# Performance work log

Hardware: AMD Instinct MI355X
Metric: run time of the kernel (lower is better)

The kernel has to match this reference:

```python
import jax, jax.numpy as jnp
import numpy as np

HEIGHT = 0.1        # height_factor
MIN_DIST = 10       # min_distance
PROM = 0.05         # prominence_factor


def _find_peaks(xn):
    """scipy.signal.find_peaks(xn, height=HEIGHT, distance=MIN_DIST,
    prominence=PROM) for a single 1D signal, vectorized.
    (Plateau handling omitted: for continuous random inputs exact ties have
    probability zero, so strict local maxima match scipy's _local_maxima_1d.)"""
    N = xn.shape[0]
    pos = jnp.arange(N)

    # 1) strict local maxima (endpoints can never be peaks in scipy)
    interior = (xn[1:-1] > xn[:-2]) & (xn[1:-1] > xn[2:])
    is_peak = jnp.pad(interior, (1, 1), constant_values=False)

    # 2) height filter
    cand = is_peak & (xn >= HEIGHT)

    # 3) distance-based greedy suppression: highest peak first, remove
    #    neighbors with |i-j| < MIN_DIST (matches _select_by_peak_distance)
    order = jnp.argsort(-xn)  # descending by value

    def step(suppressed, idx):
        keep_this = cand[idx] & ~suppressed[idx]
        near = (jnp.abs(pos - idx) < MIN_DIST) & (pos != idx)
        suppressed = suppressed | (keep_this & near)
        return suppressed, keep_this

    _, keeps = jax.lax.scan(step, jnp.zeros(N, dtype=bool), order)
    keep = jnp.zeros(N, dtype=bool).at[order].set(keeps)

    # 4) prominence (wlen=None -> full-signal base search, per position):
    #    left base  = min x over (L, i] where L = last j<i with x[j] > x[i]
    #    right base = min x over [i, R) where R = first j>i with x[j] > x[i]
    greater = xn[None, :] > xn[:, None]              # [i, j]: x_j > x_i
    left_stop = greater & (pos[None, :] < pos[:, None])
    L = jnp.max(jnp.where(left_stop, pos[None, :], -1), axis=1)
    right_stop = greater & (pos[None, :] > pos[:, None])
    R = jnp.min(jnp.where(right_stop, pos[None, :], N), axis=1)

    big = jnp.asarray(jnp.inf, xn.dtype)
    in_l = (pos[None, :] > L[:, None]) & (pos[None, :] <= pos[:, None])
    lmin = jnp.min(jnp.where(in_l, xn[None, :], big), axis=1)
    in_r = (pos[None, :] >= pos[:, None]) & (pos[None, :] < R[:, None])
    rmin = jnp.min(jnp.where(in_r, xn[None, :], big), axis=1)
    prominence = xn - jnp.maximum(lmin, rmin)

    keep = keep & (prominence >= PROM)
    return keep.astype(xn.dtype)


def setup_inputs() -> dict:
    key = jax.random.key(0)
    x = jax.random.normal(key, (16, 2048), dtype=jnp.float32)
    return {"x": x}


def reference(x):
    # per-sample min-max normalization, as in the torch module
    xmin = jnp.min(x, axis=-1, keepdims=True)
    xmax = jnp.max(x, axis=-1, keepdims=True)
    xn = (x - xmin) / (xmax - xmin + 1e-5)
    return jax.vmap(_find_peaks)(xn)
```

## Files before the change

kernel.cpp:

```cpp
#include <hip/hip_runtime.h>

#define N 2048
#define NT 256
#define EL 8
#define HEIGHTF 0.1f
#define PROMF 0.05f
#define LVLS 8

__global__ __launch_bounds__(NT)
void peak_kernel(const float* __restrict__ x, float* __restrict__ out) {
    __shared__ float xs[N];
    __shared__ float actl[16 + N + 24];
    __shared__ unsigned int nk32[3 + NT + 3];
    __shared__ float TMX[LVLS][N];
    __shared__ float TMN[LVLS][N];
    __shared__ float wred[8];
    __shared__ int wtot[4];
    __shared__ unsigned short klist[NT];
    __shared__ unsigned char keepres[N];
    __shared__ int donecnt;

    const int row = blockIdx.x;
    const int t = threadIdx.x;
    const int base = t * EL;
    const float* xr = x + row * (size_t)N;
    const int wv = t >> 6, ln = t & 63;

    float4 Ld0 = ((const float4*)(xr + base))[0];
    float4 Ld1 = ((const float4*)(xr + base))[1];
    float v0[EL] = {Ld0.x, Ld0.y, Ld0.z, Ld0.w, Ld1.x, Ld1.y, Ld1.z, Ld1.w};
    float mn = v0[0], mx = v0[0];
    #pragma unroll
    for (int e = 1; e < EL; ++e) { mn = fminf(mn, v0[e]); mx = fmaxf(mx, v0[e]); }
    #pragma unroll
    for (int off = 32; off > 0; off >>= 1) {
        mn = fminf(mn, __shfl_xor(mn, off, 64));
        mx = fmaxf(mx, __shfl_xor(mx, off, 64));
    }
    if (ln == 0) { wred[wv] = mn; wred[4 + wv] = mx; }
    nk32[t] = 0;
    if (t < 6) nk32[NT + t] = 0;
    if (t == 0) donecnt = 0;
    if (t < 16) actl[t] = -1e30f;
    if (t < 24) actl[16 + N + t] = -1e30f;
    __syncthreads();

    const float xmin = fminf(fminf(wred[0], wred[1]), fminf(wred[2], wred[3]));
    const float xmax = fmaxf(fmaxf(wred[4], wred[5]), fmaxf(wred[6], wred[7]));
    const float den = (xmax - xmin) + 1e-5f;
    float vn[EL];
    #pragma unroll
    for (int e = 0; e < EL; ++e) {
        vn[e] = (v0[e] - xmin) / den;
        xs[base + e] = vn[e];
    }
    __syncthreads();

    unsigned int undec = 0, kept = 0;
    #pragma unroll
    for (int e = 0; e < EL; ++e) {
        int i = base + e;
        float v = vn[e];
        float lf = (e == 0) ? ((i >= 1) ? xs[i-1] : 3e38f) : vn[e-1];
        float rt = (e == EL-1) ? ((i+1 < N) ? xs[i+1] : 3e38f) : vn[e+1];
        bool c = (i >= 1) && (i <= N-2) && (v > lf) && (v > rt) && (v >= HEIGHTF);
        if (c) undec |= (1u << e);
        actl[16 + i] = c ? v : -1e30f;
    }
    __syncthreads();

    float a[40];
    {
        const float4* ap = (const float4*)(actl + base);
        #pragma unroll
        for (int q = 0; q < 10; ++q) {
            float4 w = ap[q];
            a[4*q+0] = w.x; a[4*q+1] = w.y; a[4*q+2] = w.z; a[4*q+3] = w.w;
        }
    }

    auto compute_wins = [&](unsigned int ud) -> unsigned int {
        float m2v[25], m4v[23], m8v[19];
        #pragma unroll
        for (int s = 0; s < 25; ++s) m2v[s] = fmaxf(a[7+s], a[8+s]);
        #pragma unroll
        for (int s = 0; s < 23; ++s) m4v[s] = fmaxf(m2v[s], m2v[s+2]);
        #pragma unroll
        for (int s = 0; s < 19; ++s) m8v[s] = fmaxf(m4v[s], m4v[s+4]);
        unsigned int wb = 0;
        #pragma unroll
        for (int e = 0; e < EL; ++e) {
            if (ud & (1u << e)) {
                float v = a[16+e];
                float wl = fmaxf(m8v[e], a[15+e]);
                float wr = fmaxf(m8v[10+e], a[25+e]);
                if (wl < v && wr <= v) wb |= (1u << e);
            }
        }
        return wb;
    };

    {
        volatile unsigned int* nkv = nk32 + 3;
        volatile int* dcp = (volatile int*)&donecnt;
        unsigned long long lastV = ~0ULL;
        bool counted = false;
        int guard = 0;
        while (true) {
            if (undec) {
                unsigned long long V = 0;
                #pragma unroll
                for (int q = 0; q < 7; ++q)
                    V |= ((unsigned long long)(nkv[t - 3 + q] & 0xFFu)) << (8 * q);
                V <<= 1;
                if (V != lastV) {
                    lastV = V;
                    #pragma unroll
                    for (int s = 0; s < 40; ++s)
                        if ((V >> s) & 0x7FFFFULL) a[s] = -1e30f;
                    #pragma unroll
                    for (int e = 0; e < EL; ++e)
                        if (undec & (1u << e))
                            if ((V >> (16 + e)) & 0x7FFFFULL) undec &= ~(1u << e);
                    if (undec) {
                        unsigned int wb = compute_wins(undec);
                        if (wb) {
                            kept |= wb;
                            undec = 0;
                            nkv[t] = kept;
                        }
                    }
                } else {
                    __builtin_amdgcn_s_sleep(1);
                }
            }
            if (!undec && !counted) {
                nkv[t] = kept;
                __threadfence_block();
                atomicAdd(&donecnt, 1);
                counted = true;
            }
            if (*dcp >= NT) break;
            if (counted) __builtin_amdgcn_s_sleep(2);
            if (++guard > 65536) break;
        }
    }
    __syncthreads();

    float cx[EL], cn[EL];
    #pragma unroll
    for (int j = 0; j < EL; ++j) {
        int i = t + j * NT;
        float a0 = xs[i];
        bool inb = (i + 1 < N);
        float nb = inb ? xs[i + 1] : 0.0f;
        cx[j] = fmaxf(a0, inb ? nb : -3e38f);
        cn[j] = fminf(a0, inb ? nb : 3e38f);
        TMX[0][i] = cx[j];
        TMN[0][i] = cn[j];
    }
    int myc = __popc(kept);
    int pre = myc;
    #pragma unroll
    for (int off = 1; off < 64; off <<= 1) {
        int up = __shfl_up(pre, off, 64);
        if (ln >= off) pre += up;
    }
    if (ln == 63) wtot[wv] = pre;
    #pragma unroll
    for (int e = 0; e < EL; ++e) keepres[base + e] = 0;
    __syncthreads();

    {
        int woff = 0;
        #pragma unroll
        for (int w = 0; w < 4; ++w) woff += (w < wv) ? wtot[w] : 0;
        int slot = woff + pre - myc;
        #pragma unroll
        for (int e = 0; e < EL; ++e)
            if (kept & (1u << e)) klist[slot++] = (unsigned short)(base + e);
    }
    const int ktot = wtot[0] + wtot[1] + wtot[2] + wtot[3];
    #pragma unroll
    for (int pp = 0; pp < 3; ++pp) {
        const int Lv = 1 + 2 * pp;
        const int h = 1 << Lv;
        #pragma unroll
        for (int j = 0; j < EL; ++j) {
            int i = t + j * NT;
            float x1 = (i +   h < N) ? TMX[Lv-1][i+  h] : -3e38f;
            float x2 = (i + 2*h < N) ? TMX[Lv-1][i+2*h] : -3e38f;
            float x3 = (i + 3*h < N) ? TMX[Lv-1][i+3*h] : -3e38f;
            float n1 = (i +   h < N) ? TMN[Lv-1][i+  h] : 3e38f;
            float n2 = (i + 2*h < N) ? TMN[Lv-1][i+2*h] : 3e38f;
            float n3 = (i + 3*h < N) ? TMN[Lv-1][i+3*h] : 3e38f;
            float tx = fmaxf(cx[j], x1), tn = fminf(cn[j], n1);
            TMX[Lv][i] = tx;  TMN[Lv][i] = tn;
            cx[j] = fmaxf(tx, fmaxf(x2, x3));
            cn[j] = fminf(tn, fminf(n2, n3));
            TMX[Lv+1][i] = cx[j];  TMN[Lv+1][i] = cn[j];
        }
        __syncthreads();
    }
    {
        const int h = 128;
        #pragma unroll
        for (int j = 0; j < EL; ++j) {
            int i = t + j * NT;
            float x1 = (i + h < N) ? TMX[6][i+h] : -3e38f;
            float n1 = (i + h < N) ? TMN[6][i+h] : 3e38f;
            cx[j] = fmaxf(cx[j], x1);
            cn[j] = fminf(cn[j], n1);
            TMX[7][i] = cx[j];  TMN[7][i] = cn[j];
        }
        __syncthreads();
    }

    if (t < ktot) {
        const int i = klist[t];
        const float v = xs[i];
        const float* TX0 = &TMX[0][0];
        const float* TN0 = &TMN[0][0];
        int Lph = 0, Lp = i - 1, Lk = 0, Ls = 0;
        float Lm = v;
        if (Lp < 0) Lph = 2;
        int Rph = 0, Rp = i + 1, Rk = 0;
        float Rm = v;
        if (Rp >= N) Rph = 2;
        while (Lph != 2 || Rph != 2) {
            int lLev = 0, lIdx = 0, rLev = 0, rIdx = 0, Lrs = 0;
            if (Lph == 0) {
                int len = Lp + 1;
                Lk = (len >= (1 << LVLS)) ? LVLS : (31 - __clz(len));
                Ls = Lp + 1 - (1 << Lk);
                lLev = Lk - 1; lIdx = Ls;
            } else if (Lph == 1) {
                Lrs = Ls + (1 << (Lk - 1));
                lLev = Lk - 2; lIdx = Lrs;
            }
            if (Rph == 0) {
                int len = N - Rp;
                Rk = (len >= (1 << LVLS)) ? LVLS : (31 - __clz(len));
                rLev = Rk - 1; rIdx = Rp;
            } else if (Rph == 1) {
                rLev = Rk - 2; rIdx = Rp;
            }
            float lx = 0.0f, lnv = 0.0f, rx = 0.0f, rnv = 0.0f;
            if (Lph != 2) {
                const float* bX = (lLev < 0) ? xs : (TX0 + lLev * N);
                const float* bN = (lLev < 0) ? xs : (TN0 + lLev * N);
                lx = bX[lIdx]; lnv = bN[lIdx];
            }
            if (Rph != 2) {
                const float* bX = (rLev < 0) ? xs : (TX0 + rLev * N);
                const float* bN = (rLev < 0) ? xs : (TN0 + rLev * N);
                rx = bX[rIdx]; rnv = bN[rIdx];
            }
            if (Lph == 0) {
                if (lx > v) Lph = (Lk == 0) ? 2 : 1;
                else { Lm = fminf(Lm, lnv); Lp = Ls - 1; if (Lp < 0) Lph = 2; }
            } else if (Lph == 1) {
                if (lx > v) Ls = Lrs; else Lm = fminf(Lm, lnv);
                if (--Lk == 0) Lph = 2;
            }
            if (Rph == 0) {
                if (rx > v) Rph = (Rk == 0) ? 2 : 1;
                else { Rm = fminf(Rm, rnv); Rp += (1 << Rk); if (Rp >= N) Rph = 2; }
            } else if (Rph == 1) {
                if (!(rx > v)) { Rm = fminf(Rm, rnv); Rp += (1 << (Rk - 1)); }
                if (--Rk == 0) Rph = 2;
            }
        }
        if (v - fmaxf(Lm, Rm) >= PROMF) keepres[i] = 1;
    }
    __syncthreads();

    float res[EL];
    #pragma unroll
    for (int e = 0; e < EL; ++e) res[e] = keepres[base + e] ? 1.0f : 0.0f;
    float* outr = out + row * (size_t)N + base;
    ((float4*)outr)[0] = make_float4(res[0], res[1], res[2], res[3]);
    ((float4*)outr)[1] = make_float4(res[4], res[5], res[6], res[7]);
}

extern "C" void kernel_launch(void* const* d_in, const int* in_sizes, int n_in,
                              void* d_out, int out_size, void* d_ws, size_t ws_size,
                              hipStream_t stream) {
    const float* x = (const float*)d_in[0];
    float* outp = (float*)d_out;
    const int rows = in_sizes[0] / N;
    peak_kernel<<<rows, NT, 0, stream>>>(x, outp);
}
```

Measured before the change: 23.24 us.

## Resolve greedy peak suppression locally over wider window before cross-thread polling

Each thread now loads a 56-element window of candidate peaks and repeatedly finds window-local winners, meaning peaks that dominate their ±9 neighborhood, including those in neighbouring threads' ranges. It applies their suppression masks itself, so many decisions resolve without waiting for neighbour threads to publish keep bits. This is meant to cut the number of shared-memory polling rounds and sleeps in the serial dependency chain. The cost is more register pressure from the larger array and extra max-tree work per iteration, and the sleep in the polling loop is removed.

```diff
diff --git a/kernel.cpp b/kernel.cpp
--- a/kernel.cpp
+++ b/kernel.cpp
@@ -10,7 +10,7 @@
 __global__ __launch_bounds__(NT)
 void peak_kernel(const float* __restrict__ x, float* __restrict__ out) {
     __shared__ float xs[N];
-    __shared__ float actl[16 + N + 24];
+    __shared__ float actl[24 + N + 32];
     __shared__ unsigned int nk32[3 + NT + 3];
     __shared__ float TMX[LVLS][N];
     __shared__ float TMN[LVLS][N];
@@ -41,8 +41,8 @@
     nk32[t] = 0;
     if (t < 6) nk32[NT + t] = 0;
     if (t == 0) donecnt = 0;
-    if (t < 16) actl[t] = -1e30f;
-    if (t < 24) actl[16 + N + t] = -1e30f;
+    if (t < 24) actl[t] = -1e30f;
+    if (t < 32) actl[24 + N + t] = -1e30f;
     __syncthreads();
 
     const float xmin = fminf(fminf(wred[0], wred[1]), fminf(wred[2], wred[3]));
@@ -65,73 +65,99 @@
         float rt = (e == EL-1) ? ((i+1 < N) ? xs[i+1] : 3e38f) : vn[e+1];
         bool c = (i >= 1) && (i <= N-2) && (v > lf) && (v > rt) && (v >= HEIGHTF);
         if (c) undec |= (1u << e);
-        actl[16 + i] = c ? v : -1e30f;
-    }
-    __syncthreads();
-
-    float a[40];
+        actl[24 + i] = c ? v : -1e30f;
+    }
+    __syncthreads();
+
+    float a[56];
     {
         const float4* ap = (const float4*)(actl + base);
         #pragma unroll
-        for (int q = 0; q < 10; ++q) {
+        for (int q = 0; q < 14; ++q) {
             float4 w = ap[q];
             a[4*q+0] = w.x; a[4*q+1] = w.y; a[4*q+2] = w.z; a[4*q+3] = w.w;
         }
     }
 
-    auto compute_wins = [&](unsigned int ud) -> unsigned int {
-        float m2v[25], m4v[23], m8v[19];
-        #pragma unroll
-        for (int s = 0; s < 25; ++s) m2v[s] = fmaxf(a[7+s], a[8+s]);
-        #pragma unroll
-        for (int s = 0; s < 23; ++s) m4v[s] = fmaxf(m2v[s], m2v[s+2]);
-        #pragma unroll
-        for (int s = 0; s < 19; ++s) m8v[s] = fmaxf(m4v[s], m4v[s+4]);
-        unsigned int wb = 0;
+    volatile unsigned int* nkv = nk32 + 3;
+
+    auto compute_W = [&]() -> unsigned long long {
+        unsigned long long W = 0;
+        {
+            float m2[37], m4[35];
+            #pragma unroll
+            for (int s2 = 0; s2 < 37; ++s2) m2[s2] = fmaxf(a[s2], a[s2+1]);
+            #pragma unroll
+            for (int s4 = 0; s4 < 35; ++s4) m4[s4] = fmaxf(m2[s4], m2[s4+2]);
+            #pragma unroll
+            for (int s = 9; s < 28; ++s) {
+                float v = a[s];
+                float wl = fmaxf(fmaxf(m4[s-9], m4[s-5]), a[s-1]);
+                float wr = fmaxf(fmaxf(m4[s+1], m4[s+5]), a[s+9]);
+                if (wl < v && wr <= v) W |= (1ULL << s);
+            }
+        }
+        {
+            float m2[36], m4[34];
+            #pragma unroll
+            for (int s2 = 0; s2 < 36; ++s2) m2[s2] = fmaxf(a[19+s2], a[20+s2]);
+            #pragma unroll
+            for (int s4 = 0; s4 < 34; ++s4) m4[s4] = fmaxf(m2[s4], m2[s4+2]);
+            #pragma unroll
+            for (int s = 28; s < 47; ++s) {
+                float v = a[s];
+                float wl = fmaxf(fmaxf(m4[s-28], m4[s-24]), a[s-1]);
+                float wr = fmaxf(fmaxf(m4[s-18], m4[s-14]), a[s+9]);
+                if (wl < v && wr <= v) W |= (1ULL << s);
+            }
+        }
+        return W;
+    };
+
+    auto apply_mask = [&](unsigned long long Wm) {
+        #pragma unroll
+        for (int s = 0; s < 56; ++s) {
+            unsigned long long m = (s >= 9) ? ((Wm >> (s-9)) & 0x7FFFFULL)
+                                            : (Wm & ((1ULL << (s+10)) - 1));
+            if (m) a[s] = -1e30f;
+        }
+        unsigned int oldk = kept;
         #pragma unroll
         for (int e = 0; e < EL; ++e) {
-            if (ud & (1u << e)) {
-                float v = a[16+e];
-                float wl = fmaxf(m8v[e], a[15+e]);
-                float wr = fmaxf(m8v[10+e], a[25+e]);
-                if (wl < v && wr <= v) wb |= (1u << e);
-            }
-        }
-        return wb;
+            if (undec & (1u << e)) {
+                const int s = 24 + e;
+                unsigned long long w19 = (Wm >> (s-9)) & 0x7FFFFULL;
+                if ((w19 >> 9) & 1ULL) { kept |= (1u << e); undec &= ~(1u << e); }
+                else if (w19)          { undec &= ~(1u << e); }
+            }
+        }
+        if (kept != oldk) nkv[t] = kept;
     };
 
+    auto resolve = [&]() {
+        while (true) {
+            unsigned long long W = compute_W();
+            if (!W) break;
+            apply_mask(W);
+        }
+    };
+
     {
-        volatile unsigned int* nkv = nk32 + 3;
         volatile int* dcp = (volatile int*)&donecnt;
-        unsigned long long lastV = ~0ULL;
+        unsigned long long lastV = 0;
         bool counted = false;
         int guard = 0;
+        if (undec) resolve();
         while (true) {
             if (undec) {
                 unsigned long long V = 0;
                 #pragma unroll
                 for (int q = 0; q < 7; ++q)
                     V |= ((unsigned long long)(nkv[t - 3 + q] & 0xFFu)) << (8 * q);
-                V <<= 1;
                 if (V != lastV) {
                     lastV = V;
-                    #pragma unroll
-                    for (int s = 0; s < 40; ++s)
-                        if ((V >> s) & 0x7FFFFULL) a[s] = -1e30f;
-                    #pragma unroll
-                    for (int e = 0; e < EL; ++e)
-                        if (undec & (1u << e))
-                            if ((V >> (16 + e)) & 0x7FFFFULL) undec &= ~(1u << e);
-                    if (undec) {
-                        unsigned int wb = compute_wins(undec);
-                        if (wb) {
-                            kept |= wb;
-                            undec = 0;
-                            nkv[t] = kept;
-                        }
-                    }
-                } else {
-                    __builtin_amdgcn_s_sleep(1);
+                    apply_mask(V);
+                    if (undec) resolve();
                 }
             }
             if (!undec && !counted) {
```

Measured after the change: 75.80 us. 3.26x slower.

## Overlap sparse-table construction with distance-suppression spin loop using per-wave completion flags

Applied to the files above, without the earlier changes.

Interleaves building the min/max sparse-table levels with the iterative peak-distance suppression loop, so table construction fills the idle polling time instead of running as a separate phase afterwards. The block-wide atomic done counter is replaced by per-wave ballot flags. The neighbour-suppression mask is now computed with a bit dilation instead of per-bit window tests, and an initial win check is done before polling. This adds __syncthreads inside the polling loop for the first levels, which couples threads that were previously independent and could add barrier stalls.

```diff
diff --git a/kernel.cpp b/kernel.cpp
--- a/kernel.cpp
+++ b/kernel.cpp
@@ -16,9 +16,9 @@
     __shared__ float TMN[LVLS][N];
     __shared__ float wred[8];
     __shared__ int wtot[4];
+    __shared__ int wdone[4];
     __shared__ unsigned short klist[NT];
     __shared__ unsigned char keepres[N];
-    __shared__ int donecnt;
 
     const int row = blockIdx.x;
     const int t = threadIdx.x;
@@ -40,7 +40,7 @@
     if (ln == 0) { wred[wv] = mn; wred[4 + wv] = mx; }
     nk32[t] = 0;
     if (t < 6) nk32[NT + t] = 0;
-    if (t == 0) donecnt = 0;
+    if (t < 4) wdone[t] = 0;
     if (t < 16) actl[t] = -1e30f;
     if (t < 24) actl[16 + N + t] = -1e30f;
     __syncthreads();
@@ -66,87 +66,8 @@
         bool c = (i >= 1) && (i <= N-2) && (v > lf) && (v > rt) && (v >= HEIGHTF);
         if (c) undec |= (1u << e);
         actl[16 + i] = c ? v : -1e30f;
-    }
-    __syncthreads();
-
-    float a[40];
-    {
-        const float4* ap = (const float4*)(actl + base);
-        #pragma unroll
-        for (int q = 0; q < 10; ++q) {
-            float4 w = ap[q];
-            a[4*q+0] = w.x; a[4*q+1] = w.y; a[4*q+2] = w.z; a[4*q+3] = w.w;
-        }
-    }
-
-    auto compute_wins = [&](unsigned int ud) -> unsigned int {
-        float m2v[25], m4v[23], m8v[19];
-        #pragma unroll
-        for (int s = 0; s < 25; ++s) m2v[s] = fmaxf(a[7+s], a[8+s]);
-        #pragma unroll
-        for (int s = 0; s < 23; ++s) m4v[s] = fmaxf(m2v[s], m2v[s+2]);
-        #pragma unroll
-        for (int s = 0; s < 19; ++s) m8v[s] = fmaxf(m4v[s], m4v[s+4]);
-        unsigned int wb = 0;
-        #pragma unroll
-        for (int e = 0; e < EL; ++e) {
-            if (ud & (1u << e)) {
-                float v = a[16+e];
-                float wl = fmaxf(m8v[e], a[15+e]);
-                float wr = fmaxf(m8v[10+e], a[25+e]);
-                if (wl < v && wr <= v) wb |= (1u << e);
-            }
-        }
-        return wb;
-    };
-
-    {
-        volatile unsigned int* nkv = nk32 + 3;
-        volatile int* dcp = (volatile int*)&donecnt;
-        unsigned long long lastV = ~0ULL;
-        bool counted = false;
-        int guard = 0;
-        while (true) {
-            if (undec) {
-                unsigned long long V = 0;
-                #pragma unroll
-                for (int q = 0; q < 7; ++q)
-                    V |= ((unsigned long long)(nkv[t - 3 + q] & 0xFFu)) << (8 * q);
-                V <<= 1;
-                if (V != lastV) {
-                    lastV = V;
-                    #pragma unroll
-                    for (int s = 0; s < 40; ++s)
-                        if ((V >> s) & 0x7FFFFULL) a[s] = -1e30f;
-                    #pragma unroll
-                    for (int e = 0; e < EL; ++e)
-                        if (undec & (1u << e))
-                            if ((V >> (16 + e)) & 0x7FFFFULL) undec &= ~(1u << e);
-                    if (undec) {
-                        unsigned int wb = compute_wins(undec);
-                        if (wb) {
-                            kept |= wb;
-                            undec = 0;
-                            nkv[t] = kept;
-                        }
-                    }
-                } else {
-                    __builtin_amdgcn_s_sleep(1);
-                }
-            }
-            if (!undec && !counted) {
-                nkv[t] = kept;
-                __threadfence_block();
-                atomicAdd(&donecnt, 1);
-                counted = true;
-            }
-            if (*dcp >= NT) break;
-            if (counted) __builtin_amdgcn_s_sleep(2);
-            if (++guard > 65536) break;
-        }
-    }
-    __syncthreads();
-
+        keepres[i] = 0;
+    }
     float cx[EL], cn[EL];
     #pragma unroll
     for (int j = 0; j < EL; ++j) {
@@ -159,6 +80,107 @@
         TMX[0][i] = cx[j];
         TMN[0][i] = cn[j];
     }
+    __syncthreads();
+
+    float a[40];
+    {
+        const float4* ap = (const float4*)(actl + base);
+        #pragma unroll
+        for (int q = 0; q < 10; ++q) {
+            float4 w = ap[q];
+            a[4*q+0] = w.x; a[4*q+1] = w.y; a[4*q+2] = w.z; a[4*q+3] = w.w;
+        }
+    }
+
+    auto compute_wins = [&](unsigned int ud) -> unsigned int {
+        float m2v[25], m4v[23], m8v[19];
+        #pragma unroll
+        for (int s = 0; s < 25; ++s) m2v[s] = fmaxf(a[7+s], a[8+s]);
+        #pragma unroll
+        for (int s = 0; s < 23; ++s) m4v[s] = fmaxf(m2v[s], m2v[s+2]);
+        #pragma unroll
+        for (int s = 0; s < 19; ++s) m8v[s] = fmaxf(m4v[s], m4v[s+4]);
+        unsigned int wb = 0;
+        #pragma unroll
+        for (int e = 0; e < EL; ++e) {
+            if (ud & (1u << e)) {
+                float v = a[16+e];
+                float wl = fmaxf(m8v[e], a[15+e]);
+                float wr = fmaxf(m8v[10+e], a[25+e]);
+                if (wl < v && wr <= v) wb |= (1u << e);
+            }
+        }
+        return wb;
+    };
+
+    auto dilate9 = [](unsigned long long m) -> unsigned long long {
+        m |= (m << 1) | (m >> 1);
+        m |= (m << 2) | (m >> 2);
+        m |= (m << 3) | (m >> 3);
+        m |= (m << 3) | (m >> 3);
+        return m;
+    };
+
+    {
+        volatile unsigned int* nkv = nk32 + 3;
+        unsigned long long lastV = 0;
+        int lvl = 1;
+        int guard = 0;
+        if (undec) {
+            unsigned int wb = compute_wins(undec);
+            if (wb) { kept |= wb; undec = 0; nkv[t] = kept; }
+        }
+        while (true) {
+            if (undec) {
+                unsigned long long V = 0;
+                #pragma unroll
+                for (int q = 0; q < 7; ++q)
+                    V |= ((unsigned long long)(nkv[t - 3 + q] & 0xFFu)) << (8 * q);
+                if (V != lastV) {
+                    lastV = V;
+                    unsigned long long D = dilate9(V);
+                    #pragma unroll
+                    for (int s = 0; s < 40; ++s)
+                        if ((D >> (s + 8)) & 1ULL) a[s] = -1e30f;
+                    #pragma unroll
+                    for (int e = 0; e < EL; ++e)
+                        if (undec & (1u << e))
+                            if ((D >> (24 + e)) & 1ULL) undec &= ~(1u << e);
+                    if (undec) {
+                        unsigned int wb = compute_wins(undec);
+                        if (wb) { kept |= wb; undec = 0; nkv[t] = kept; }
+                    }
+                }
+            }
+            if (lvl < LVLS) {
+                const int h = 1 << lvl;
+                #pragma unroll
+                for (int j = 0; j < EL; ++j) {
+                    int i = t + j * NT;
+                    bool inb = (i + h < N);
+                    float bx = inb ? TMX[lvl-1][i+h] : -3e38f;
+                    float bn = inb ? TMN[lvl-1][i+h] : 3e38f;
+                    cx[j] = fmaxf(cx[j], bx);
+                    cn[j] = fminf(cn[j], bn);
+                    TMX[lvl][i] = cx[j];
+                    TMN[lvl][i] = cn[j];
+                }
+                ++lvl;
+                __syncthreads();
+                continue;
+            }
+            bool mydone = (undec == 0);
+            unsigned long long bal = __ballot(mydone);
+            if (bal == ~0ULL && ln == 0) ((volatile int*)wdone)[wv] = 1;
+            volatile int* wd = (volatile int*)wdone;
+            int d0 = wd[0], d1 = wd[1], d2 = wd[2], d3 = wd[3];
+            if (d0 & d1 & d2 & d3) break;
+            if (mydone) __builtin_amdgcn_s_sleep(1);
+            if (++guard > 65536) break;
+        }
+    }
+    __syncthreads();
+
     int myc = __popc(kept);
     int pre = myc;
     #pragma unroll
@@ -167,10 +189,7 @@
         if (ln >= off) pre += up;
     }
     if (ln == 63) wtot[wv] = pre;
-    #pragma unroll
-    for (int e = 0; e < EL; ++e) keepres[base + e] = 0;
-    __syncthreads();
-
+    __syncthreads();
     {
         int woff = 0;
         #pragma unroll
@@ -181,40 +200,7 @@
             if (kept & (1u << e)) klist[slot++] = (unsigned short)(base + e);
     }
     const int ktot = wtot[0] + wtot[1] + wtot[2] + wtot[3];
-    #pragma unroll
-    for (int pp = 0; pp < 3; ++pp) {
-        const int Lv = 1 + 2 * pp;
-        const int h = 1 << Lv;
-        #pragma unroll
-        for (int j = 0; j < EL; ++j) {
-            int i = t + j * NT;
-            float x1 = (i +   h < N) ? TMX[Lv-1][i+  h] : -3e38f;
-            float x2 = (i + 2*h < N) ? TMX[Lv-1][i+2*h] : -3e38f;
-            float x3 = (i + 3*h < N) ? TMX[Lv-1][i+3*h] : -3e38f;
-            float n1 = (i +   h < N) ? TMN[Lv-1][i+  h] : 3e38f;
-            float n2 = (i + 2*h < N) ? TMN[Lv-1][i+2*h] : 3e38f;
-            float n3 = (i + 3*h < N) ? TMN[Lv-1][i+3*h] : 3e38f;
-            float tx = fmaxf(cx[j], x1), tn = fminf(cn[j], n1);
-            TMX[Lv][i] = tx;  TMN[Lv][i] = tn;
-            cx[j] = fmaxf(tx, fmaxf(x2, x3));
-            cn[j] = fminf(tn, fminf(n2, n3));
-            TMX[Lv+1][i] = cx[j];  TMN[Lv+1][i] = cn[j];
-        }
-        __syncthreads();
-    }
-    {
-        const int h = 128;
-        #pragma unroll
-        for (int j = 0; j < EL; ++j) {
-            int i = t + j * NT;
-            float x1 = (i + h < N) ? TMX[6][i+h] : -3e38f;
-            float n1 = (i + h < N) ? TMN[6][i+h] : 3e38f;
-            cx[j] = fmaxf(cx[j], x1);
-            cn[j] = fminf(cn[j], n1);
-            TMX[7][i] = cx[j];  TMN[7][i] = cn[j];
-        }
-        __syncthreads();
-    }
+    __syncthreads();
 
     if (t < ktot) {
         const int i = klist[t];
```

New measurement: 23.70 us. No clear change (+2.0%).
